# Optimization experiments

Measured on AMD Instinct MI355X. Metric: run time of the kernel, lower is better.

## Reference

```python
import jax, jax.numpy as jnp
import numpy as np


def _conv(x, w, b, padding='SAME' if False else 'VALID'):
    # NCHW conv, OIHW weights
    out = jax.lax.conv_general_dilated(
        x, w, window_strides=(1, 1), padding=padding,
        dimension_numbers=('NCHW', 'OIHW', 'NCHW'))
    return out + b[None, :, None, None]


def setup_inputs() -> dict:
    key = jax.random.key(0)
    ks = jax.random.split(key, 14)
    s = lambda k, shape, scale=0.1: jax.random.normal(k, shape, dtype=jnp.float32) * scale
    return {
        'x': jax.random.normal(ks[0], (8, 16, 512, 512), dtype=jnp.float32),
        'y': jax.random.normal(ks[1], (8, 5, 512, 512), dtype=jnp.float32),
        'fuse_w': s(ks[2], (16, 5, 1, 1)),
        'fuse_b': s(ks[3], (16,)),
        'se_w1': s(ks[4], (16, 16)),
        'se_w2': s(ks[5], (5, 16)),
        'bd_w': s(ks[6], (2, 5, 1, 1)),
        'bd_b': s(ks[7], (2,)),
        'fc_w': s(ks[8], (16, 32, 3, 3)),
        'fc_b': s(ks[9], (16,)),
        'fm_w': s(ks[10], (2, 16, 1, 1)),
        'fm_b': s(ks[11], (2,)),
        'cv_w': s(ks[12], (16, 1, 1, 1)),
        'cv_b': s(ks[13], (16,)),
    }


def reference(x, y, fuse_w, fuse_b, se_w1, se_w2, bd_w, bd_b,
              fc_w, fc_b, fm_w, fm_b, cv_w, cv_b):
    # fuse: 1x1 conv 5->16 + ReLU
    fuse_box = jax.nn.relu(_conv(y, fuse_w, fuse_b, 'VALID'))  # [B,16,H,W]
    # global average pool -> SE mimic MLP -> sigmoid gate over 5 channels
    gap = jnp.mean(fuse_box, axis=(2, 3))                       # [B,16]
    se = jax.nn.sigmoid(jax.nn.relu(gap @ se_w1.T) @ se_w2.T)   # [B,5]
    feat_se = y * se[:, :, None, None]                          # [B,5,H,W]
    # boundary head: 1x1 conv 5->2, softmax over channel, take fg prob
    boundary = _conv(feat_se, bd_w, bd_b, 'VALID')              # [B,2,H,W]
    boundary_scale = jax.nn.softmax(boundary, axis=1)[:, 1:2]   # [B,1,H,W]
    # mask head: concat(x, fuse_box) -> 3x3 conv 32->16 + ReLU -> 1x1 conv 16->2
    feat_concat = jnp.concatenate([x, fuse_box], axis=1)        # [B,32,H,W]
    fcc = jax.nn.relu(_conv(feat_concat, fc_w, fc_b, 'SAME'))   # [B,16,H,W]
    mask = _conv(fcc, fm_w, fm_b, 'VALID')                      # [B,2,H,W]
    mask_scale = jax.nn.softmax(mask, axis=1)[:, 1:2]           # [B,1,H,W]
    # fused scale factor, clamp, expand to 16 channels via 1x1 conv
    scalefactor = jnp.clip(mask_scale + boundary_scale, 0.0, 1.0)
    return _conv(scalefactor, cv_w, cv_b, 'VALID')              # [B,16,H,W]
```

## Files before the change

kernel.cpp:

```cpp
#include <hip/hip_runtime.h>
#include <hip/hip_bf16.h>

#define HW 262144
#define IW 512
#define TW 64
#define TH 8
#define HLW 66
#define NHALO 660
#define ROWU 40

typedef __attribute__((ext_vector_type(8))) short short8;
typedef __attribute__((ext_vector_type(4))) float f32x4;
typedef __attribute__((ext_vector_type(4))) unsigned int uint4v;

static __device__ inline unsigned int bpack2(float a, float b) {
  __hip_bfloat16 ha = __float2bfloat16(a);
  __hip_bfloat16 hb = __float2bfloat16(b);
  unsigned short ua = *reinterpret_cast<unsigned short*>(&ha);
  unsigned short ub = *reinterpret_cast<unsigned short*>(&hb);
  return (unsigned int)ua | ((unsigned int)ub << 16);
}

__global__ __launch_bounds__(256) void k_gap(
    const float* __restrict__ y, const float* __restrict__ fuse_w,
    const float* __restrict__ fuse_b, float* __restrict__ partial) {
  __shared__ float fw[80], fb[16];
  __shared__ float red[4][16];
  int tid = threadIdx.x;
  if (tid < 80) fw[tid] = fuse_w[tid];
  if (tid < 16) fb[tid] = fuse_b[tid];
  __syncthreads();

  int b = blockIdx.x >> 7, chunk = blockIdx.x & 127;
  const float* yb = y + (size_t)b * 5 * HW + chunk * 2048;

  float sums[16];
#pragma unroll
  for (int o = 0; o < 16; ++o) sums[o] = 0.f;

#pragma unroll
  for (int i = 0; i < 2048; i += 1024) {
    int p = i + tid * 4;
    f32x4 yv[5];
#pragma unroll
    for (int c = 0; c < 5; ++c)
      yv[c] = *reinterpret_cast<const f32x4*>(&yb[(size_t)c * HW + p]);
#pragma unroll
    for (int o = 0; o < 16; ++o) {
#pragma unroll
      for (int j = 0; j < 4; ++j) {
        float a = fb[o];
#pragma unroll
        for (int c = 0; c < 5; ++c) a = fmaf(fw[o * 5 + c], yv[c][j], a);
        sums[o] += fmaxf(a, 0.f);
      }
    }
  }

  int lane = tid & 63, wv = tid >> 6;
#pragma unroll
  for (int o = 0; o < 16; ++o) {
    float v = sums[o];
    for (int off = 32; off > 0; off >>= 1) v += __shfl_down(v, off);
    if (lane == 0) red[wv][o] = v;
  }
  __syncthreads();
  if (tid < 16)
    partial[blockIdx.x * 16 + tid] =
        red[0][tid] + red[1][tid] + red[2][tid] + red[3][tid];
}

__global__ __launch_bounds__(256) void k_se2(
    const float* __restrict__ partial, const float* __restrict__ se_w1,
    const float* __restrict__ se_w2, const float* __restrict__ bd_w,
    const float* __restrict__ fc_w, float* __restrict__ bd_eff,
    unsigned short* __restrict__ wTab) {
  int tid = threadIdx.x;
  {
    int b = tid >> 5, sub = tid & 31;
    float g[16];
#pragma unroll
    for (int c = 0; c < 16; ++c) g[c] = 0.f;
#pragma unroll
    for (int k = 0; k < 4; ++k) {
      const float* p = partial + (b * 128 + sub + k * 32) * 16;
#pragma unroll
      for (int c = 0; c < 16; ++c) g[c] += p[c];
    }
#pragma unroll
    for (int c = 0; c < 16; ++c) {
      float v = g[c];
      v += __shfl_xor(v, 1);  v += __shfl_xor(v, 2);
      v += __shfl_xor(v, 4);  v += __shfl_xor(v, 8);
      v += __shfl_xor(v, 16);
      g[c] = v * (1.f / 262144.f);
    }
    if (sub == 0) {
      float h[16];
#pragma unroll
      for (int j = 0; j < 16; ++j) {
        float s = 0.f;
#pragma unroll
        for (int c = 0; c < 16; ++c) s += g[c] * se_w1[j * 16 + c];
        h[j] = fmaxf(s, 0.f);
      }
#pragma unroll
      for (int i = 0; i < 5; ++i) {
        float s = 0.f;
#pragma unroll
        for (int j = 0; j < 16; ++j) s += h[j] * se_w2[i * 16 + j];
        float se = 1.f / (1.f + expf(-s));
        bd_eff[b * 10 + i]     = bd_w[i] * se;
        bd_eff[b * 10 + 5 + i] = bd_w[5 + i] * se;
      }
    }
  }
  for (int i = tid; i < 4608; i += 256) {
    int ci = i & 31, rest = i >> 5;
    int oc = rest & 15, s = rest >> 4;
    float v = fc_w[(oc * 32 + ci) * 9 + s];
    __hip_bfloat16 h = __float2bfloat16(v);
    wTab[i] = *reinterpret_cast<unsigned short*>(&h);
  }
}

__global__ __launch_bounds__(256) void k_main8(
    const float* __restrict__ x, const float* __restrict__ y,
    const float* __restrict__ fuse_w, const float* __restrict__ fuse_b,
    const unsigned short* __restrict__ wTab,
    const float* __restrict__ bd_eff, const float* __restrict__ bd_b,
    const float* __restrict__ fc_b,
    const float* __restrict__ fm_w, const float* __restrict__ fm_b,
    const float* __restrict__ cv_w, const float* __restrict__ cv_b,
    float* __restrict__ out) {
  __shared__ unsigned short tile[NHALO * ROWU];
  __shared__ float s_fw[80], s_fb[16], s_bde[10], s_bdb[2], s_fm[32],
      s_fmb[2], s_cv[16], s_cvb[16], s_fcb[16];

  int tid = threadIdx.x;
  int bsel = blockIdx.z;
  int h0 = blockIdx.y * TH;
  int w0 = blockIdx.x * TW;

  if (tid < 80) s_fw[tid] = fuse_w[tid];
  else if (tid < 96)  s_fb[tid - 80]   = fuse_b[tid - 80];
  else if (tid < 106) s_bde[tid - 96]  = bd_eff[bsel * 10 + tid - 96];
  else if (tid < 108) s_bdb[tid - 106] = bd_b[tid - 106];
  else if (tid < 140) s_fm[tid - 108]  = fm_w[tid - 108];
  else if (tid < 142) s_fmb[tid - 140] = fm_b[tid - 140];
  else if (tid < 158) s_cv[tid - 142]  = cv_w[tid - 142];
  else if (tid < 174) s_cvb[tid - 158] = cv_b[tid - 158];
  else if (tid < 190) s_fcb[tid - 174] = fc_b[tid - 174];

  int lane = tid & 63, wv = tid >> 6;
  int l15 = lane & 15, q = lane >> 4;

  short8 afrag[9];
#pragma unroll
  for (int s = 0; s < 9; ++s)
    afrag[s] = *reinterpret_cast<const short8*>(wTab + (s * 16 + l15) * 32 + q * 8);

  __syncthreads();

  const float* yb = y + (size_t)bsel * 5 * HW;
  const float* xb = x + (size_t)bsel * 16 * HW;

  if (tid < 180) {
    int r = tid / 18, s = tid - r * 18;
    int gh = h0 - 1 + r;
    bool rowv = (gh >= 0) & (gh < IW);
    if (s > 0 && s < 17) {
      int col0 = 1 + (s - 1) * 4;
      int p0 = r * HLW + col0;
      int gw0 = w0 + (s - 1) * 4;
      if (rowv) {
        const float* xrow = xb + (size_t)gh * IW + gw0;
        const float* yrow = yb + (size_t)gh * IW + gw0;
        unsigned uu[4][4];
#pragma unroll
        for (int half = 0; half < 2; ++half) {
#pragma unroll
          for (int cp = 0; cp < 4; ++cp) {
            int c = half * 8 + cp * 2;
            f32x4 va = *reinterpret_cast<const f32x4*>(xrow + (size_t)c * HW);
            f32x4 vb =
                *reinterpret_cast<const f32x4*>(xrow + (size_t)(c + 1) * HW);
#pragma unroll
            for (int j = 0; j < 4; ++j) uu[j][cp] = bpack2(va[j], vb[j]);
          }
#pragma unroll
          for (int j = 0; j < 4; ++j) {
            uint4v* dst = reinterpret_cast<uint4v*>(&tile[(p0 + j) * ROWU]);
            dst[half] = uint4v{uu[j][0], uu[j][1], uu[j][2], uu[j][3]};
          }
        }
        f32x4 yv[5];
#pragma unroll
        for (int c = 0; c < 5; ++c)
          yv[c] = *reinterpret_cast<const f32x4*>(yrow + (size_t)c * HW);
#pragma unroll
        for (int half = 0; half < 2; ++half) {
#pragma unroll
          for (int op = 0; op < 4; ++op) {
            int o = half * 8 + op * 2;
#pragma unroll
            for (int j = 0; j < 4; ++j) {
              float a0 = s_fb[o], a1 = s_fb[o + 1];
#pragma unroll
              for (int c = 0; c < 5; ++c) {
                a0 = fmaf(s_fw[o * 5 + c], yv[c][j], a0);
                a1 = fmaf(s_fw[(o + 1) * 5 + c], yv[c][j], a1);
              }
              uu[j][op] = bpack2(fmaxf(a0, 0.f), fmaxf(a1, 0.f));
            }
          }
#pragma unroll
          for (int j = 0; j < 4; ++j) {
            uint4v* dst = reinterpret_cast<uint4v*>(&tile[(p0 + j) * ROWU]);
            dst[2 + half] = uint4v{uu[j][0], uu[j][1], uu[j][2], uu[j][3]};
          }
        }
#pragma unroll
        for (int j = 0; j < 4; ++j) {
          float bl0 = s_bdb[0], bl1 = s_bdb[1];
#pragma unroll
          for (int c = 0; c < 5; ++c) {
            bl0 = fmaf(s_bde[c], yv[c][j], bl0);
            bl1 = fmaf(s_bde[5 + c], yv[c][j], bl1);
          }
          *reinterpret_cast<float*>(&tile[(p0 + j) * ROWU + 32]) =
              1.f / (1.f + __expf(bl0 - bl1));
        }
      } else {
        uint4v z = {0, 0, 0, 0};
#pragma unroll
        for (int j = 0; j < 4; ++j) {
          uint4v* dst = reinterpret_cast<uint4v*>(&tile[(p0 + j) * ROWU]);
          dst[0] = z; dst[1] = z; dst[2] = z; dst[3] = z;
          *reinterpret_cast<float*>(&tile[(p0 + j) * ROWU + 32]) = 0.f;
        }
      }
    } else {
      int col = (s == 0) ? 0 : 65;
      int p = r * HLW + col;
      int gw = w0 - 1 + col;
      bool valid = rowv & (gw >= 0) & (gw < IW);
      uint4v* dst = reinterpret_cast<uint4v*>(&tile[p * ROWU]);
      if (valid) {
        int gofs = gh * IW + gw;
        {
          float a0 = xb[gofs],          a1 = xb[HW + gofs];
          float a2 = xb[2 * HW + gofs], a3 = xb[3 * HW + gofs];
          float a4 = xb[4 * HW + gofs], a5 = xb[5 * HW + gofs];
          float a6 = xb[6 * HW + gofs], a7 = xb[7 * HW + gofs];
          dst[0] = uint4v{bpack2(a0, a1), bpack2(a2, a3),
                          bpack2(a4, a5), bpack2(a6, a7)};
        }
        {
          float a0 = xb[8 * HW + gofs],  a1 = xb[9 * HW + gofs];
          float a2 = xb[10 * HW + gofs], a3 = xb[11 * HW + gofs];
          float a4 = xb[12 * HW + gofs], a5 = xb[13 * HW + gofs];
          float a6 = xb[14 * HW + gofs], a7 = xb[15 * HW + gofs];
          dst[1] = uint4v{bpack2(a0, a1), bpack2(a2, a3),
                          bpack2(a4, a5), bpack2(a6, a7)};
        }
        float yv[5];
#pragma unroll
        for (int c = 0; c < 5; ++c) yv[c] = yb[c * HW + gofs];
        float fo[8];
#pragma unroll
        for (int o = 0; o < 8; ++o) {
          float a = s_fb[o];
#pragma unroll
          for (int c = 0; c < 5; ++c) a = fmaf(s_fw[o * 5 + c], yv[c], a);
          fo[o] = fmaxf(a, 0.f);
        }
        dst[2] = uint4v{bpack2(fo[0], fo[1]), bpack2(fo[2], fo[3]),
                        bpack2(fo[4], fo[5]), bpack2(fo[6], fo[7])};
#pragma unroll
        for (int o = 0; o < 8; ++o) {
          float a = s_fb[8 + o];
#pragma unroll
          for (int c = 0; c < 5; ++c) a = fmaf(s_fw[(8 + o) * 5 + c], yv[c], a);
          fo[o] = fmaxf(a, 0.f);
        }
        dst[3] = uint4v{bpack2(fo[0], fo[1]), bpack2(fo[2], fo[3]),
                        bpack2(fo[4], fo[5]), bpack2(fo[6], fo[7])};
        float bl0 = s_bdb[0], bl1 = s_bdb[1];
#pragma unroll
        for (int c = 0; c < 5; ++c) {
          bl0 = fmaf(s_bde[c], yv[c], bl0);
          bl1 = fmaf(s_bde[5 + c], yv[c], bl1);
        }
        *reinterpret_cast<float*>(&tile[p * ROWU + 32]) =
            1.f / (1.f + __expf(bl0 - bl1));
      } else {
        uint4v z = {0, 0, 0, 0};
        dst[0] = z; dst[1] = z; dst[2] = z; dst[3] = z;
        *reinterpret_cast<float*>(&tile[p * ROWU + 32]) = 0.f;
      }
    }
  }
  __syncthreads();

  const char* tb = reinterpret_cast<const char*>(tile);
  unsigned bofs[8];
  f32x4 acc[8];
#pragma unroll
  for (int g = 0; g < 8; ++g) {
    int row = 2 * wv + (g >> 2), c0 = (g & 3) * 16;
    bofs[g] = (unsigned)((row * HLW + c0 + l15) * (ROWU * 2) + q * 16);
    acc[g] = f32x4{0.f, 0.f, 0.f, 0.f};
  }
#pragma unroll
  for (int kh = 0; kh < 3; ++kh) {
#pragma unroll
    for (int kw = 0; kw < 3; ++kw) {
      short8 a = afrag[kh * 3 + kw];
#pragma unroll
      for (int g = 0; g < 8; ++g) {
        short8 bfr = *reinterpret_cast<const short8*>(
            tb + bofs[g] + (kh * HLW + kw) * (ROWU * 2));
        acc[g] = __builtin_amdgcn_mfma_f32_16x16x32_bf16(a, bfr, acc[g], 0, 0, 0);
      }
    }
  }

  float pm0[8], pm1[8];
#pragma unroll
  for (int g = 0; g < 8; ++g) {
    float p0 = 0.f, p1 = 0.f;
#pragma unroll
    for (int j = 0; j < 4; ++j) {
      int oc = q * 4 + j;
      float fv = fmaxf(acc[g][j] + s_fcb[oc], 0.f);
      p0 = fmaf(s_fm[oc], fv, p0);
      p1 = fmaf(s_fm[16 + oc], fv, p1);
    }
    pm0[g] = p0; pm1[g] = p1;
  }
#pragma unroll
  for (int g = 0; g < 8; ++g) pm0[g] += __shfl_xor(pm0[g], 16);
#pragma unroll
  for (int g = 0; g < 8; ++g) pm1[g] += __shfl_xor(pm1[g], 16);
#pragma unroll
  for (int g = 0; g < 8; ++g) pm0[g] += __shfl_xor(pm0[g], 32);
#pragma unroll
  for (int g = 0; g < 8; ++g) pm1[g] += __shfl_xor(pm1[g], 32);

  float* outb = out + (size_t)bsel * 16 * HW;
#pragma unroll
  for (int g = 0; g < 8; ++g) {
    int row = 2 * wv + (g >> 2), c0 = (g & 3) * 16;
    int gofs = (h0 + row) * IW + w0 + c0 + l15;
    float mscale =
        1.f / (1.f + __expf((pm0[g] + s_fmb[0]) - (pm1[g] + s_fmb[1])));
    float bsc = *reinterpret_cast<const float*>(
        tb + ((row + 1) * HLW + c0 + l15 + 1) * (ROWU * 2) + 64);
    float sc = fminf(fmaxf(mscale + bsc, 0.f), 1.f);
#pragma unroll
    for (int j = 0; j < 4; ++j) {
      int oc = q * 4 + j;
      outb[(size_t)oc * HW + gofs] = fmaf(s_cv[oc], sc, s_cvb[oc]);
    }
  }
}

extern "C" void kernel_launch(void* const* d_in, const int* in_sizes, int n_in,
                              void* d_out, int out_size, void* d_ws, size_t ws_size,
                              hipStream_t stream) {
  const float* x      = (const float*)d_in[0];
  const float* y      = (const float*)d_in[1];
  const float* fuse_w = (const float*)d_in[2];
  const float* fuse_b = (const float*)d_in[3];
  const float* se_w1  = (const float*)d_in[4];
  const float* se_w2  = (const float*)d_in[5];
  const float* bd_w   = (const float*)d_in[6];
  const float* bd_b   = (const float*)d_in[7];
  const float* fc_w   = (const float*)d_in[8];
  const float* fc_b   = (const float*)d_in[9];
  const float* fm_w   = (const float*)d_in[10];
  const float* fm_b   = (const float*)d_in[11];
  const float* cv_w   = (const float*)d_in[12];
  const float* cv_b   = (const float*)d_in[13];
  float* out = (float*)d_out;

  char* ws = (char*)d_ws;
  float* partial = (float*)ws;
  float* bd_eff  = partial + 1024 * 16;
  unsigned short* wTab = (unsigned short*)(ws + 65856);

  k_gap<<<1024, 256, 0, stream>>>(y, fuse_w, fuse_b, partial);
  k_se2<<<1, 256, 0, stream>>>(partial, se_w1, se_w2, bd_w, fc_w, bd_eff,
                               wTab);
  k_main8<<<dim3(8, 64, 8), 256, 0, stream>>>(
      x, y, fuse_w, fuse_b, wTab, bd_eff, bd_b, fc_b, fm_w, fm_b, cv_w, cv_b,
      out);
}
```

Before: 123.0 us.

## Split 16-channel output expansion into separate vectorized kernel and swizzle block order

The main conv kernel now writes only the single-channel clamped scale factor to a workspace buffer. A new elementwise kernel reads it and writes all 16 output channels with float4 stores. This replaces the scattered 16-lane-wide scalar stores in the conv kernel. The conv grid is also flattened with a block-index swizzle that interleaves batches across consecutive blocks. The cost is an extra launch and an extra round trip of the scale map through memory.

```diff
diff --git a/kernel.cpp b/kernel.cpp
--- a/kernel.cpp
+++ b/kernel.cpp
@@ -124,23 +124,24 @@
   }
 }
 
-__global__ __launch_bounds__(256) void k_main8(
+__global__ __launch_bounds__(256) void k_conv9(
     const float* __restrict__ x, const float* __restrict__ y,
     const float* __restrict__ fuse_w, const float* __restrict__ fuse_b,
     const unsigned short* __restrict__ wTab,
     const float* __restrict__ bd_eff, const float* __restrict__ bd_b,
     const float* __restrict__ fc_b,
     const float* __restrict__ fm_w, const float* __restrict__ fm_b,
-    const float* __restrict__ cv_w, const float* __restrict__ cv_b,
-    float* __restrict__ out) {
+    float* __restrict__ scP) {
   __shared__ unsigned short tile[NHALO * ROWU];
   __shared__ float s_fw[80], s_fb[16], s_bde[10], s_bdb[2], s_fm[32],
-      s_fmb[2], s_cv[16], s_cvb[16], s_fcb[16];
+      s_fmb[2], s_fcb[16];
 
   int tid = threadIdx.x;
-  int bsel = blockIdx.z;
-  int h0 = blockIdx.y * TH;
-  int w0 = blockIdx.x * TW;
+  int bid = blockIdx.x;
+  int swz = (bid & 7) * 512 + (bid >> 3);
+  int bx = swz & 7, by = (swz >> 3) & 63, bsel = swz >> 9;
+  int h0 = by * TH;
+  int w0 = bx * TW;
 
   if (tid < 80) s_fw[tid] = fuse_w[tid];
   else if (tid < 96)  s_fb[tid - 80]   = fuse_b[tid - 80];
@@ -148,9 +149,7 @@
   else if (tid < 108) s_bdb[tid - 106] = bd_b[tid - 106];
   else if (tid < 140) s_fm[tid - 108]  = fm_w[tid - 108];
   else if (tid < 142) s_fmb[tid - 140] = fm_b[tid - 140];
-  else if (tid < 158) s_cv[tid - 142]  = cv_w[tid - 142];
-  else if (tid < 174) s_cvb[tid - 158] = cv_b[tid - 158];
-  else if (tid < 190) s_fcb[tid - 174] = fc_b[tid - 174];
+  else if (tid < 158) s_fcb[tid - 142] = fc_b[tid - 142];
 
   int lane = tid & 63, wv = tid >> 6;
   int l15 = lane & 15, q = lane >> 4;
@@ -348,7 +347,7 @@
 #pragma unroll
   for (int g = 0; g < 8; ++g) pm1[g] += __shfl_xor(pm1[g], 32);
 
-  float* outb = out + (size_t)bsel * 16 * HW;
+  float* scb = scP + (size_t)bsel * HW;
 #pragma unroll
   for (int g = 0; g < 8; ++g) {
     int row = 2 * wv + (g >> 2), c0 = (g & 3) * 16;
@@ -358,11 +357,30 @@
     float bsc = *reinterpret_cast<const float*>(
         tb + ((row + 1) * HLW + c0 + l15 + 1) * (ROWU * 2) + 64);
     float sc = fminf(fmaxf(mscale + bsc, 0.f), 1.f);
-#pragma unroll
-    for (int j = 0; j < 4; ++j) {
-      int oc = q * 4 + j;
-      outb[(size_t)oc * HW + gofs] = fmaf(s_cv[oc], sc, s_cvb[oc]);
-    }
+    if (q == 0) scb[gofs] = sc;
+  }
+}
+
+__global__ __launch_bounds__(256) void k_expand(
+    const float* __restrict__ scP, const float* __restrict__ cv_w,
+    const float* __restrict__ cv_b, float* __restrict__ out) {
+  __shared__ float s_cv[16], s_cvb[16];
+  int tid = threadIdx.x;
+  if (tid < 16) s_cv[tid] = cv_w[tid];
+  else if (tid < 32) s_cvb[tid - 16] = cv_b[tid - 16];
+  __syncthreads();
+
+  int idx = blockIdx.x * 256 + tid;
+  int b = idx >> 16;
+  int px4 = idx & 65535;
+  f32x4 sv = *reinterpret_cast<const f32x4*>(&scP[(size_t)b * HW + px4 * 4]);
+  float* ob = out + (size_t)b * 16 * HW + (size_t)px4 * 4;
+#pragma unroll
+  for (int oc = 0; oc < 16; ++oc) {
+    float cw = s_cv[oc], cb = s_cvb[oc];
+    f32x4 ov = {fmaf(cw, sv[0], cb), fmaf(cw, sv[1], cb),
+                fmaf(cw, sv[2], cb), fmaf(cw, sv[3], cb)};
+    *reinterpret_cast<f32x4*>(ob + (size_t)oc * HW) = ov;
   }
 }
 
@@ -389,11 +407,12 @@
   float* partial = (float*)ws;
   float* bd_eff  = partial + 1024 * 16;
   unsigned short* wTab = (unsigned short*)(ws + 65856);
+  float* scP = (float*)(ws + 75264);
 
   k_gap<<<1024, 256, 0, stream>>>(y, fuse_w, fuse_b, partial);
   k_se2<<<1, 256, 0, stream>>>(partial, se_w1, se_w2, bd_w, fc_w, bd_eff,
                                wTab);
-  k_main8<<<dim3(8, 64, 8), 256, 0, stream>>>(
-      x, y, fuse_w, fuse_b, wTab, bd_eff, bd_b, fc_b, fm_w, fm_b, cv_w, cv_b,
-      out);
-}
+  k_conv9<<<4096, 256, 0, stream>>>(x, y, fuse_w, fuse_b, wTab, bd_eff, bd_b,
+                                    fc_b, fm_w, fm_b, scP);
+  k_expand<<<2048, 256, 0, stream>>>(scP, cv_w, cv_b, out);
+}
```

Result: slower. 126.2 us (+2.6%).
